# Performance work log

Hardware: AMD Instinct MI355X
Metric: run time of the kernel (lower is better)

The kernel has to match this reference:

```python
import jax, jax.numpy as jnp
import numpy as np

D = 256          # d_embed
KD = 256         # key_d_embed
NHEAD = 8
DK = D // NHEAD  # 32
QH = QW = 128
QWS = 16
KH = KW = 64
KWS = 8
R = QWS // KWS   # qk_ratio = 2
SCALE = 1.0 / np.sqrt(DK)


def _rel_index():
    # query coords on fine grid, key coords scaled up by ratio R
    qc = np.stack(np.meshgrid(np.arange(QWS), np.arange(QWS), indexing='ij'), -1).reshape(-1, 2)
    kc = np.stack(np.meshgrid(np.arange(KWS), np.arange(KWS), indexing='ij'), -1).reshape(-1, 2) * R
    rel = qc[:, None, :] - kc[None, :, :] + (QWS - R)  # values in [0, 2*QWS-R-1]
    return jnp.asarray(rel[..., 0] * (2 * QWS - R) + rel[..., 1])  # (QWS^2, KWS^2)


def _partition(t, ws):
    # (B, h, H, W, d) -> (B, h, H/ws, W/ws, ws*ws, d)
    B, h, H, W, d = t.shape
    t = t.reshape(B, h, H // ws, ws, W // ws, ws, d).transpose(0, 1, 2, 4, 3, 5, 6)
    return t.reshape(B, h, H // ws, W // ws, ws * ws, d)


def _merge(t, ws, H, W):
    # inverse of _partition
    B, h, nH, nW, _, d = t.shape
    t = t.reshape(B, h, nH, nW, ws, ws, d).transpose(0, 1, 2, 4, 3, 5, 6)
    return t.reshape(B, h, H, W, d)


def setup_inputs() -> dict:
    key = jax.random.key(0)
    ks = jax.random.split(key, 9)
    x = jax.random.normal(ks[0], (8, QH, QW, D), dtype=jnp.float32)
    z = jax.random.normal(ks[1], (8, KH, KW, KD), dtype=jnp.float32)
    mask = jax.random.randint(ks[2], (1, NHEAD, QH // QWS, QW // QWS, QWS * QWS, KWS * KWS), 0, 2) == 1
    Wq = jax.random.normal(ks[3], (D, D), dtype=jnp.float32) * 0.02
    bq = jnp.zeros((D,), dtype=jnp.float32)
    Wkv = jax.random.normal(ks[4], (KD, 2 * D), dtype=jnp.float32) * 0.02
    bkv = jnp.zeros((2 * D,), dtype=jnp.float32)
    Wo = jax.random.normal(ks[5], (D, D), dtype=jnp.float32) * 0.02
    bo = jnp.zeros((D,), dtype=jnp.float32)
    rel_table = jax.random.normal(ks[6], ((2 * QWS - R) ** 2, NHEAD), dtype=jnp.float32) * 0.02
    return {"x": x, "z": z, "mask": mask, "Wq": Wq, "bq": bq, "Wkv": Wkv, "bkv": bkv, "Wo": Wo, "bo": bo, "rel_table": rel_table}


def reference(x, z, mask, Wq, bq, Wkv, bkv, Wo, bo, rel_table):
    B, H, W, _ = x.shape
    q = (x @ Wq + bq).reshape(B, H, W, NHEAD, DK).transpose(0, 3, 1, 2, 4)        # (B,h,H,W,dk)
    kv = (z @ Wkv + bkv).reshape(B, KH, KW, 2, NHEAD, DK).transpose(3, 0, 4, 1, 2, 5)
    k, v = kv[0], kv[1]                                                           # (B,h,_H,_W,dk)
    sq, sk = QWS // 2, KWS // 2
    q = jnp.roll(q, (-sq, -sq), axis=(2, 3))
    k = jnp.roll(k, (-sk, -sk), axis=(2, 3))
    v = jnp.roll(v, (-sk, -sk), axis=(2, 3))
    q = _partition(q, QWS)   # (B,h,nh,nw,QWS^2,dk)
    k = _partition(k, KWS)   # (B,h,nh,nw,KWS^2,dk)
    v = _partition(v, KWS)
    attn = jnp.einsum('bhnmqd,bhnmkd->bhnmqk', q, k) * SCALE
    bias = rel_table[_rel_index()].transpose(2, 0, 1)[None, :, None, None]        # (1,h,1,1,QWS^2,KWS^2)
    attn = attn + bias
    attn = jnp.where(mask, jnp.float32(-1e9), attn)
    attn = jax.nn.softmax(attn, axis=-1)
    out = jnp.einsum('bhnmqk,bhnmkd->bhnmqd', attn, v)
    out = _merge(out, QWS, H, W)
    out = jnp.roll(out, (sq, sq), axis=(2, 3))
    out = out.transpose(0, 2, 3, 1, 4).reshape(B, H, W, D)
    return out @ Wo + bo
```

## Files before the change

### kernel.cpp

```cpp
#include <hip/hip_runtime.h>
#include <hip/hip_bf16.h>
#include <type_traits>


typedef __attribute__((ext_vector_type(8))) short short8v;
typedef __attribute__((ext_vector_type(4))) float f32x4;
typedef __attribute__((ext_vector_type(8))) unsigned short ushort8v;
typedef __attribute__((ext_vector_type(4))) unsigned short ushort4v;

#define DEV __device__ __forceinline__

DEV unsigned short f2bf(float f) {
    union { float f; unsigned u; } v; v.f = f;
    unsigned r = v.u + 0x7FFFu + ((v.u >> 16) & 1u);
    return (unsigned short)(r >> 16);
}

#define ATT_SCALE 0.17677669529663687f

__global__ void prep_weights(const float* __restrict__ Wq, const float* __restrict__ Wkv,
                             const float* __restrict__ Wo,
                             unsigned short* __restrict__ WqT, unsigned short* __restrict__ WkvT,
                             unsigned short* __restrict__ WoT) {
    int idx = blockIdx.x * 256 + threadIdx.x;
    if (idx < 65536) {
        int n = idx >> 8, k = idx & 255;
        WqT[idx] = f2bf(Wq[k * 256 + n] * ATT_SCALE);
    } else if (idx < 196608) {
        int i = idx - 65536;
        int n = i >> 8, k = i & 255;
        WkvT[i] = f2bf(Wkv[k * 512 + n]);
    } else {
        int i = idx - 196608;
        int n = i >> 8, k = i & 255;
        WoT[i] = f2bf(Wo[k * 256 + n]);
    }
}

__global__ void prep_bias(const float* __restrict__ rel_table, const float* __restrict__ bq,
                          float* __restrict__ biasb, float* __restrict__ bqs) {
    int idx = blockIdx.x * 256 + threadIdx.x;
    if (idx < 131072) {
        int head = idx >> 14;
        int q = (idx >> 6) & 255;
        int k = idx & 63;
        int qi = q >> 4, qj = q & 15;
        int ki = k >> 3, kj = k & 7;
        int r0 = qi - 2 * ki + 14, r1 = qj - 2 * kj + 14;
        biasb[idx] = rel_table[(r0 * 30 + r1) * 8 + head];
    } else if (idx < 131328) {
        int i = idx - 131072;
        bqs[i] = bq[i] * ATT_SCALE;
    }
}

__global__ void prep_mask(const int* __restrict__ mask, unsigned long long* __restrict__ mp) {
    int idx = blockIdx.x * 256 + threadIdx.x;
    const int4* src = reinterpret_cast<const int4*>(mask + (size_t)idx * 64);
    unsigned long long bits = 0;
#pragma unroll
    for (int c = 0; c < 16; ++c) {
        int4 v = src[c];
        if (v.x) bits |= 1ull << (c * 4 + 0);
        if (v.y) bits |= 1ull << (c * 4 + 1);
        if (v.z) bits |= 1ull << (c * 4 + 2);
        if (v.w) bits |= 1ull << (c * 4 + 3);
    }
    mp[idx] = bits;
}

template <bool AF32, bool OUT_BF16>
__global__ __launch_bounds__(256) void gemm_proj(
    const void* __restrict__ Ain, const unsigned short* __restrict__ BT,
    const float* __restrict__ bias, void* __restrict__ Cout,
    int M, int N, int K)
{
    __shared__ __align__(16) unsigned char As[2][8192];
    __shared__ __align__(16) unsigned char Bs[2][8192];
    const float* Af = (const float*)Ain;
    const unsigned short* Ab = (const unsigned short*)Ain;

    const int tid = threadIdx.x;
    const int mb = blockIdx.y * 128, nb = blockIdx.x * 128;
    const int w = tid >> 6, lane = tid & 63, lr = lane & 15, lg = lane >> 4;
    const int wm = (w >> 1) * 64, wn = (w & 1) * 64;

    const int cr0 = (w << 5) + (lane >> 2);
    const int csp = lane & 3;
    const int cs0 = csp ^ ((cr0 >> 1) & 3);
    const int cs1 = csp ^ (((cr0 + 16) >> 1) & 3);

    auto stageB = [&](int buf, int kb) {
        __builtin_amdgcn_global_load_lds(
            (const __attribute__((address_space(1))) void*)(BT + (size_t)(nb + cr0) * K + kb + cs0 * 8),
            (__attribute__((address_space(3))) void*)(&Bs[buf][w << 11]), 16, 0, 0);
        __builtin_amdgcn_global_load_lds(
            (const __attribute__((address_space(1))) void*)(BT + (size_t)(nb + cr0 + 16) * K + kb + cs1 * 8),
            (__attribute__((address_space(3))) void*)(&Bs[buf][(w << 11) + 1024]), 16, 0, 0);
    };
    auto stageA_lds = [&](int buf, int kb) {
        __builtin_amdgcn_global_load_lds(
            (const __attribute__((address_space(1))) void*)(Ab + (size_t)(mb + cr0) * K + kb + cs0 * 8),
            (__attribute__((address_space(3))) void*)(&As[buf][w << 11]), 16, 0, 0);
        __builtin_amdgcn_global_load_lds(
            (const __attribute__((address_space(1))) void*)(Ab + (size_t)(mb + cr0 + 16) * K + kb + cs1 * 8),
            (__attribute__((address_space(3))) void*)(&As[buf][(w << 11) + 1024]), 16, 0, 0);
    };

    float4 areg[2][2];
    auto loadA = [&](int kb) {
#pragma unroll
        for (int i = 0; i < 2; ++i) {
            int flat = tid + (i << 8);
            int r = flat >> 2, sp = flat & 3;
            int s = sp ^ ((r >> 1) & 3);
            const float* src = Af + (size_t)(mb + r) * K + kb + s * 8;
            areg[i][0] = *reinterpret_cast<const float4*>(src);
            areg[i][1] = *reinterpret_cast<const float4*>(src + 4);
        }
    };
    auto writeA = [&](int buf) {
#pragma unroll
        for (int i = 0; i < 2; ++i) {
            int flat = tid + (i << 8);
            int r = flat >> 2, sp = flat & 3;
            ushort8v u = { f2bf(areg[i][0].x), f2bf(areg[i][0].y),
                           f2bf(areg[i][0].z), f2bf(areg[i][0].w),
                           f2bf(areg[i][1].x), f2bf(areg[i][1].y),
                           f2bf(areg[i][1].z), f2bf(areg[i][1].w) };
            *reinterpret_cast<ushort8v*>(&As[buf][r * 64 + sp * 16]) = u;
        }
    };

    auto rdA = [&](int buf, int row) -> short8v {
        int swz = (lg ^ ((row >> 1) & 3)) << 4;
        return *reinterpret_cast<const short8v*>(&As[buf][row * 64 + swz]);
    };
    auto rdB = [&](int buf, int row) -> short8v {
        int swz = (lg ^ ((row >> 1) & 3)) << 4;
        return *reinterpret_cast<const short8v*>(&Bs[buf][row * 64 + swz]);
    };

    f32x4 acc[4][4];
#pragma unroll
    for (int i = 0; i < 4; ++i)
#pragma unroll
        for (int j = 0; j < 4; ++j) acc[i][j] = {0.f, 0.f, 0.f, 0.f};

    if constexpr (AF32) { loadA(0); stageB(0, 0); writeA(0); }
    else               { stageA_lds(0, 0); stageB(0, 0); }
    __syncthreads();

    const int NT = K >> 5;
    int cur = 0;
    for (int t = 0; t < NT; ++t) {
        if (t + 1 < NT) {
            if constexpr (AF32) { loadA((t + 1) << 5); stageB(cur ^ 1, (t + 1) << 5); }
            else { stageA_lds(cur ^ 1, (t + 1) << 5); stageB(cur ^ 1, (t + 1) << 5); }
        }
        short8v af[4], bfr[4];
#pragma unroll
        for (int mt = 0; mt < 4; ++mt) af[mt] = rdA(cur, wm + mt * 16 + lr);
#pragma unroll
        for (int nt = 0; nt < 4; ++nt) bfr[nt] = rdB(cur, wn + nt * 16 + lr);
#pragma unroll
        for (int mt = 0; mt < 4; ++mt)
#pragma unroll
            for (int nt = 0; nt < 4; ++nt)
                acc[mt][nt] = __builtin_amdgcn_mfma_f32_16x16x32_bf16(
                    af[mt], bfr[nt], acc[mt][nt], 0, 0, 0);
        if (t + 1 < NT) { if constexpr (AF32) writeA(cur ^ 1); }
        __syncthreads();
        cur ^= 1;
    }

#pragma unroll
    for (int mt = 0; mt < 4; ++mt)
#pragma unroll
        for (int nt = 0; nt < 4; ++nt)
#pragma unroll
            for (int j = 0; j < 4; ++j) {
                int row = mb + wm + mt * 16 + lg * 4 + j;
                int col = nb + wn + nt * 16 + lr;
                float v = acc[mt][nt][j] + bias[col];
                if constexpr (OUT_BF16)
                    ((unsigned short*)Cout)[(size_t)row * N + col] = f2bf(v);
                else
                    ((float*)Cout)[(size_t)row * N + col] = v;
            }
}

__global__ __launch_bounds__(256) void win_attn(
    unsigned short* __restrict__ Qbuf,
    const unsigned short* __restrict__ KVbuf,
    const unsigned long long* __restrict__ maskp,
    const float* __restrict__ biasb)
{
    __shared__ __align__(16) unsigned char Pb[256 * 128];
    __shared__ __align__(16) unsigned short Vt[32][72];

    const int tid = threadIdx.x;
    const int win = blockIdx.x, head = blockIdx.y, b = blockIdx.z;
    const int wi = win >> 3, wj = win & 7;
    const int w = tid >> 6, lane = tid & 63, lr = lane & 15, lg = lane >> 4;
    const int qb = w * 64;

    {
        int key = tid & 63, c = tid >> 6;
        int kr = (wi * 8 + (key >> 3) + 4) & 63;
        int kc = (wj * 8 + (key & 7) + 4) & 63;
        ushort8v v = *reinterpret_cast<const ushort8v*>(
            KVbuf + ((size_t)(b * 4096 + kr * 64 + kc)) * 512 + 256 + head * 32 + c * 8);
#pragma unroll
        for (int e = 0; e < 8; ++e) Vt[c * 8 + e][key] = v[e];
    }

    short8v qf[4], kf[4];
#pragma unroll
    for (int mt = 0; mt < 4; ++mt) {
        int q = qb + mt * 16 + lr;
        int gr = (wi * 16 + (q >> 4) + 8) & 127;
        int gc = (wj * 16 + (q & 15) + 8) & 127;
        qf[mt] = *reinterpret_cast<const short8v*>(
            Qbuf + ((size_t)(b * 16384 + gr * 128 + gc)) * 256 + head * 32 + lg * 8);
    }
#pragma unroll
    for (int nt = 0; nt < 4; ++nt) {
        int key = nt * 16 + lr;
        int kr = (wi * 8 + (key >> 3) + 4) & 63;
        int kc = (wj * 8 + (key & 7) + 4) & 63;
        kf[nt] = *reinterpret_cast<const short8v*>(
            KVbuf + ((size_t)(b * 4096 + kr * 64 + kc)) * 512 + head * 32 + lg * 8);
    }

    f32x4 s[4][4];
#pragma unroll
    for (int mt = 0; mt < 4; ++mt)
#pragma unroll
        for (int nt = 0; nt < 4; ++nt) s[mt][nt] = {0.f, 0.f, 0.f, 0.f};
    __builtin_amdgcn_s_setprio(1);
#pragma unroll
    for (int mt = 0; mt < 4; ++mt)
#pragma unroll
        for (int nt = 0; nt < 4; ++nt)
            s[mt][nt] = __builtin_amdgcn_mfma_f32_16x16x32_bf16(qf[mt], kf[nt], s[mt][nt], 0, 0, 0);
    __builtin_amdgcn_s_setprio(0);

    const unsigned long long* mrow = maskp + (size_t)(head * 64 + win) * 256;
#pragma unroll
    for (int mt = 0; mt < 4; ++mt) {
#pragma unroll
        for (int j = 0; j < 4; ++j) {
            int q = qb + mt * 16 + lg * 4 + j;
            unsigned long long mb = mrow[q];
            const float* brow = biasb + (size_t)(head * 256 + q) * 64;
            float v[4];
            float m = -3.0e38f;
#pragma unroll
            for (int nt = 0; nt < 4; ++nt) {
                int key = nt * 16 + lr;
                float sv = s[mt][nt][j] + brow[key];
                if ((mb >> key) & 1ull) sv = -1.0e9f;
                v[nt] = sv;
                m = fmaxf(m, sv);
            }
#pragma unroll
            for (int d = 1; d < 16; d <<= 1) m = fmaxf(m, __shfl_xor(m, d, 64));
            float sum = 0.f;
#pragma unroll
            for (int nt = 0; nt < 4; ++nt) { v[nt] = __expf(v[nt] - m); sum += v[nt]; }
#pragma unroll
            for (int d = 1; d < 16; d <<= 1) sum += __shfl_xor(sum, d, 64);
            float inv = 1.0f / sum;
            int sw = (q & 7) << 4;
#pragma unroll
            for (int nt = 0; nt < 4; ++nt) {
                int off = q * 128 + (((nt * 16 + lr) * 2) ^ sw);
                *reinterpret_cast<unsigned short*>(Pb + off) = f2bf(v[nt] * inv);
            }
        }
    }

    __syncthreads();

    f32x4 o[4][2];
#pragma unroll
    for (int mt = 0; mt < 4; ++mt)
#pragma unroll
        for (int nt = 0; nt < 2; ++nt) o[mt][nt] = {0.f, 0.f, 0.f, 0.f};
#pragma unroll
    for (int kc = 0; kc < 2; ++kc) {
        short8v pf[4], vf[2];
#pragma unroll
        for (int mt = 0; mt < 4; ++mt) {
            int row = qb + mt * 16 + lr;
            int coff = (kc * 64 + lg * 16) ^ ((row & 7) << 4);
            pf[mt] = *reinterpret_cast<const short8v*>(Pb + row * 128 + coff);
        }
#pragma unroll
        for (int nt = 0; nt < 2; ++nt)
            vf[nt] = *reinterpret_cast<const short8v*>(&Vt[nt * 16 + lr][kc * 32 + lg * 8]);
        __builtin_amdgcn_s_setprio(1);
#pragma unroll
        for (int mt = 0; mt < 4; ++mt)
#pragma unroll
            for (int nt = 0; nt < 2; ++nt)
                o[mt][nt] = __builtin_amdgcn_mfma_f32_16x16x32_bf16(pf[mt], vf[nt], o[mt][nt], 0, 0, 0);
        __builtin_amdgcn_s_setprio(0);
    }

#pragma unroll
    for (int mt = 0; mt < 4; ++mt)
#pragma unroll
        for (int j = 0; j < 4; ++j) {
            int q = qb + mt * 16 + lg * 4 + j;
            int gr = (wi * 16 + (q >> 4) + 8) & 127;
            int gc = (wj * 16 + (q & 15) + 8) & 127;
            unsigned short* dst =
                Qbuf + ((size_t)(b * 16384 + gr * 128 + gc)) * 256 + head * 32;
#pragma unroll
            for (int nt = 0; nt < 2; ++nt)
                dst[nt * 16 + lr] = f2bf(o[mt][nt][j]);
        }
}

extern "C" void kernel_launch(void* const* d_in, const int* in_sizes, int n_in,
                              void* d_out, int out_size, void* d_ws, size_t ws_size,
                              hipStream_t stream) {
    const float* x    = (const float*)d_in[0];
    const float* z    = (const float*)d_in[1];
    const int*   mask = (const int*)d_in[2];
    const float* Wq   = (const float*)d_in[3];
    const float* bq   = (const float*)d_in[4];
    const float* Wkv  = (const float*)d_in[5];
    const float* bkv  = (const float*)d_in[6];
    const float* Wo   = (const float*)d_in[7];
    const float* bo   = (const float*)d_in[8];
    const float* rel  = (const float*)d_in[9];
    float* out = (float*)d_out;

    char* ws = (char*)d_ws;
    unsigned short*     Qbuf  = (unsigned short*)(ws);
    unsigned short*     KVbuf = (unsigned short*)(ws + 67108864);
    unsigned short*     WqT   = (unsigned short*)(ws + 100663296);
    unsigned short*     WkvT  = (unsigned short*)(ws + 100794368);
    unsigned short*     WoT   = (unsigned short*)(ws + 101056512);
    float*              biasb = (float*)(ws + 101187584);
    unsigned long long* maskp = (unsigned long long*)(ws + 101711872);
    float*              bqs   = (float*)(ws + 102760448);

    prep_weights<<<1024, 256, 0, stream>>>(Wq, Wkv, Wo, WqT, WkvT, WoT);
    prep_bias<<<513, 256, 0, stream>>>(rel, bq, biasb, bqs);
    prep_mask<<<512, 256, 0, stream>>>(mask, maskp);

    gemm_proj<true, true><<<dim3(2, 1024), 256, 0, stream>>>(
        (const void*)x, WqT, bqs, (void*)Qbuf, 131072, 256, 256);
    gemm_proj<true, true><<<dim3(4, 256), 256, 0, stream>>>(
        (const void*)z, WkvT, bkv, (void*)KVbuf, 32768, 512, 256);
    win_attn<<<dim3(64, 8, 8), 256, 0, stream>>>(Qbuf, KVbuf, maskp, biasb);
    gemm_proj<false, false><<<dim3(2, 1024), 256, 0, stream>>>(
        (const void*)Qbuf, WoT, bo, (void*)out, 131072, 256, 256);
}
```

Before: 221.3 us.

## Fuse Q projection, window attention and output projection into one kernel

```diff
diff --git a/kernel.cpp b/kernel.cpp
--- a/kernel.cpp
+++ b/kernel.cpp
@@ -7,6 +7,7 @@
 typedef __attribute__((ext_vector_type(4))) float f32x4;
 typedef __attribute__((ext_vector_type(8))) unsigned short ushort8v;
 typedef __attribute__((ext_vector_type(4))) unsigned short ushort4v;
+typedef unsigned long long u64;
 
 #define DEV __device__ __forceinline__
 
@@ -14,6 +15,22 @@
     union { float f; unsigned u; } v; v.f = f;
     unsigned r = v.u + 0x7FFFu + ((v.u >> 16) & 1u);
     return (unsigned short)(r >> 16);
+}
+
+DEV short8v cvt_f32x8(const float4 lo, const float4 hi) {
+    union U { __hip_bfloat162 h[4]; short8v s; } u;
+    u.h[0] = __float22bfloat162_rn(float2{lo.x, lo.y});
+    u.h[1] = __float22bfloat162_rn(float2{lo.z, lo.w});
+    u.h[2] = __float22bfloat162_rn(float2{hi.x, hi.y});
+    u.h[3] = __float22bfloat162_rn(float2{hi.z, hi.w});
+    return u.s;
+}
+
+DEV uint2 pack4(f32x4 v) {
+    union { __hip_bfloat162 h; unsigned u; } a, b;
+    a.h = __float22bfloat162_rn(float2{v[0], v[1]});
+    b.h = __float22bfloat162_rn(float2{v[2], v[3]});
+    return uint2{a.u, b.u};
 }
 
 #define ATT_SCALE 0.17677669529663687f
@@ -54,10 +71,10 @@
     }
 }
 
-__global__ void prep_mask(const int* __restrict__ mask, unsigned long long* __restrict__ mp) {
+__global__ void prep_mask(const int* __restrict__ mask, u64* __restrict__ mp) {
     int idx = blockIdx.x * 256 + threadIdx.x;
     const int4* src = reinterpret_cast<const int4*>(mask + (size_t)idx * 64);
-    unsigned long long bits = 0;
+    u64 bits = 0;
 #pragma unroll
     for (int c = 0; c < 16; ++c) {
         int4 v = src[c];
@@ -69,16 +86,13 @@
     mp[idx] = bits;
 }
 
-template <bool AF32, bool OUT_BF16>
-__global__ __launch_bounds__(256) void gemm_proj(
-    const void* __restrict__ Ain, const unsigned short* __restrict__ BT,
-    const float* __restrict__ bias, void* __restrict__ Cout,
+__global__ __launch_bounds__(256) void gemm_kv(
+    const float* __restrict__ Af, const unsigned short* __restrict__ BT,
+    const float* __restrict__ bias, unsigned short* __restrict__ Cout,
     int M, int N, int K)
 {
     __shared__ __align__(16) unsigned char As[2][8192];
     __shared__ __align__(16) unsigned char Bs[2][8192];
-    const float* Af = (const float*)Ain;
-    const unsigned short* Ab = (const unsigned short*)Ain;
 
     const int tid = threadIdx.x;
     const int mb = blockIdx.y * 128, nb = blockIdx.x * 128;
@@ -98,14 +112,6 @@
             (const __attribute__((address_space(1))) void*)(BT + (size_t)(nb + cr0 + 16) * K + kb + cs1 * 8),
             (__attribute__((address_space(3))) void*)(&Bs[buf][(w << 11) + 1024]), 16, 0, 0);
     };
-    auto stageA_lds = [&](int buf, int kb) {
-        __builtin_amdgcn_global_load_lds(
-            (const __attribute__((address_space(1))) void*)(Ab + (size_t)(mb + cr0) * K + kb + cs0 * 8),
-            (__attribute__((address_space(3))) void*)(&As[buf][w << 11]), 16, 0, 0);
-        __builtin_amdgcn_global_load_lds(
-            (const __attribute__((address_space(1))) void*)(Ab + (size_t)(mb + cr0 + 16) * K + kb + cs1 * 8),
-            (__attribute__((address_space(3))) void*)(&As[buf][(w << 11) + 1024]), 16, 0, 0);
-    };
 
     float4 areg[2][2];
     auto loadA = [&](int kb) {
@@ -131,7 +137,6 @@
             *reinterpret_cast<ushort8v*>(&As[buf][r * 64 + sp * 16]) = u;
         }
     };
-
     auto rdA = [&](int buf, int row) -> short8v {
         int swz = (lg ^ ((row >> 1) & 3)) << 4;
         return *reinterpret_cast<const short8v*>(&As[buf][row * 64 + swz]);
@@ -147,17 +152,13 @@
 #pragma unroll
         for (int j = 0; j < 4; ++j) acc[i][j] = {0.f, 0.f, 0.f, 0.f};
 
-    if constexpr (AF32) { loadA(0); stageB(0, 0); writeA(0); }
-    else               { stageA_lds(0, 0); stageB(0, 0); }
+    loadA(0); stageB(0, 0); writeA(0);
     __syncthreads();
 
     const int NT = K >> 5;
     int cur = 0;
     for (int t = 0; t < NT; ++t) {
-        if (t + 1 < NT) {
-            if constexpr (AF32) { loadA((t + 1) << 5); stageB(cur ^ 1, (t + 1) << 5); }
-            else { stageA_lds(cur ^ 1, (t + 1) << 5); stageB(cur ^ 1, (t + 1) << 5); }
-        }
+        if (t + 1 < NT) { loadA((t + 1) << 5); stageB(cur ^ 1, (t + 1) << 5); }
         short8v af[4], bfr[4];
 #pragma unroll
         for (int mt = 0; mt < 4; ++mt) af[mt] = rdA(cur, wm + mt * 16 + lr);
@@ -169,7 +170,7 @@
             for (int nt = 0; nt < 4; ++nt)
                 acc[mt][nt] = __builtin_amdgcn_mfma_f32_16x16x32_bf16(
                     af[mt], bfr[nt], acc[mt][nt], 0, 0, 0);
-        if (t + 1 < NT) { if constexpr (AF32) writeA(cur ^ 1); }
+        if (t + 1 < NT) writeA(cur ^ 1);
         __syncthreads();
         cur ^= 1;
     }
@@ -182,146 +183,204 @@
             for (int j = 0; j < 4; ++j) {
                 int row = mb + wm + mt * 16 + lg * 4 + j;
                 int col = nb + wn + nt * 16 + lr;
-                float v = acc[mt][nt][j] + bias[col];
-                if constexpr (OUT_BF16)
-                    ((unsigned short*)Cout)[(size_t)row * N + col] = f2bf(v);
-                else
-                    ((float*)Cout)[(size_t)row * N + col] = v;
+                Cout[(size_t)row * N + col] = f2bf(acc[mt][nt][j] + bias[col]);
             }
 }
 
-__global__ __launch_bounds__(256) void win_attn(
-    unsigned short* __restrict__ Qbuf,
-    const unsigned short* __restrict__ KVbuf,
-    const unsigned long long* __restrict__ maskp,
-    const float* __restrict__ biasb)
+__global__ __launch_bounds__(256, 2) void fused_attn(
+    const float* __restrict__ x, const unsigned short* __restrict__ KVbuf,
+    const unsigned short* __restrict__ WqT, const unsigned short* __restrict__ WoT,
+    const float* __restrict__ bqs, const float* __restrict__ bo,
+    const u64* __restrict__ maskp, const float* __restrict__ biasb,
+    float* __restrict__ out)
 {
-    __shared__ __align__(16) unsigned char Pb[256 * 128];
-    __shared__ __align__(16) unsigned short Vt[32][72];
+    __shared__ __align__(16) unsigned char L[73728];
 
     const int tid = threadIdx.x;
-    const int win = blockIdx.x, head = blockIdx.y, b = blockIdx.z;
+    const int w = tid >> 6, lane = tid & 63, lr = lane & 15, lg = lane >> 4;
+    const int qblk = blockIdx.x, win = blockIdx.y, b = blockIdx.z;
     const int wi = win >> 3, wj = win & 7;
-    const int w = tid >> 6, lane = tid & 63, lr = lane & 15, lg = lane >> 4;
-    const int qb = w * 64;
 
     {
         int key = tid & 63, c = tid >> 6;
         int kr = (wi * 8 + (key >> 3) + 4) & 63;
         int kc = (wj * 8 + (key & 7) + 4) & 63;
-        ushort8v v = *reinterpret_cast<const ushort8v*>(
-            KVbuf + ((size_t)(b * 4096 + kr * 64 + kc)) * 512 + 256 + head * 32 + c * 8);
-#pragma unroll
-        for (int e = 0; e < 8; ++e) Vt[c * 8 + e][key] = v[e];
-    }
-
-    short8v qf[4], kf[4];
-#pragma unroll
-    for (int mt = 0; mt < 4; ++mt) {
-        int q = qb + mt * 16 + lr;
-        int gr = (wi * 16 + (q >> 4) + 8) & 127;
-        int gc = (wj * 16 + (q & 15) + 8) & 127;
-        qf[mt] = *reinterpret_cast<const short8v*>(
-            Qbuf + ((size_t)(b * 16384 + gr * 128 + gc)) * 256 + head * 32 + lg * 8);
-    }
+        const unsigned short* vsrc =
+            KVbuf + ((size_t)(b * 4096 + kr * 64 + kc)) * 512 + 256 + c * 64;
+        unsigned char* vt = L + 32768 + (key >> 5) * 16384;
+        const int klby = (key & 31) * 2;
+#pragma unroll
+        for (int i = 0; i < 8; ++i) {
+            ushort8v v = *reinterpret_cast<const ushort8v*>(vsrc + i * 8);
+#pragma unroll
+            for (int e = 0; e < 8; ++e) {
+                int d = c * 64 + i * 8 + e;
+                *reinterpret_cast<unsigned short*>(
+                    vt + d * 64 + (klby ^ (((d >> 1) & 3) << 4))) = (unsigned short)v[e];
+            }
+        }
+    }
+
+    f32x4 acc[16];
+#pragma unroll
+    for (int i = 0; i < 16; ++i) acc[i] = {0.f, 0.f, 0.f, 0.f};
+
+    const unsigned short* wqb = WqT + (size_t)(w * 64 + lr) * 256 + lg * 8;
+    const float* xr[4];
+#pragma unroll
+    for (int qt = 0; qt < 4; ++qt) {
+        int gr = (wi * 16 + qblk * 4 + qt + 8) & 127;
+        int gc = (wj * 16 + lr + 8) & 127;
+        xr[qt] = x + ((size_t)((b * 128 + gr) * 128 + gc)) * 256 + lg * 8;
+    }
+#pragma unroll
+    for (int kt = 0; kt < 8; ++kt) {
+        short8v wqf[4], xf[4];
+#pragma unroll
+        for (int nt = 0; nt < 4; ++nt)
+            wqf[nt] = *reinterpret_cast<const short8v*>(wqb + nt * 4096 + kt * 32);
+#pragma unroll
+        for (int qt = 0; qt < 4; ++qt) {
+            float4 lo = *reinterpret_cast<const float4*>(xr[qt] + kt * 32);
+            float4 hi = *reinterpret_cast<const float4*>(xr[qt] + kt * 32 + 4);
+            xf[qt] = cvt_f32x8(lo, hi);
+        }
+#pragma unroll
+        for (int nt = 0; nt < 4; ++nt)
+#pragma unroll
+            for (int qt = 0; qt < 4; ++qt)
+                acc[nt * 4 + qt] = __builtin_amdgcn_mfma_f32_16x16x32_bf16(
+                    wqf[nt], xf[qt], acc[nt * 4 + qt], 0, 0, 0);
+    }
+#pragma unroll
+    for (int nt = 0; nt < 4; ++nt) {
+        int n0 = w * 64 + nt * 16 + lg * 4;
+        f32x4 bq4 = *reinterpret_cast<const f32x4*>(bqs + n0);
+        unsigned char* pl = L + (w * 2 + (nt >> 1)) * 4096;
+        int cby = (nt & 1) * 32 + lg * 8;
+#pragma unroll
+        for (int qt = 0; qt < 4; ++qt) {
+            int qr = qt * 16 + lr;
+            uint2 pk = pack4(acc[nt * 4 + qt] + bq4);
+            *reinterpret_cast<uint2*>(pl + qr * 64 + (cby ^ (((qr >> 1) & 3) << 4))) = pk;
+        }
+    }
+    __syncthreads();
+
+    const int qrow = w * 16 + lr;
+    const int qg = qblk * 64 + qrow;
+    const int swzq = ((qrow >> 1) & 3) << 4;
+    const unsigned short* kp[4];
 #pragma unroll
     for (int nt = 0; nt < 4; ++nt) {
         int key = nt * 16 + lr;
         int kr = (wi * 8 + (key >> 3) + 4) & 63;
         int kc = (wj * 8 + (key & 7) + 4) & 63;
-        kf[nt] = *reinterpret_cast<const short8v*>(
-            KVbuf + ((size_t)(b * 4096 + kr * 64 + kc)) * 512 + head * 32 + lg * 8);
-    }
-
-    f32x4 s[4][4];
-#pragma unroll
-    for (int mt = 0; mt < 4; ++mt)
-#pragma unroll
-        for (int nt = 0; nt < 4; ++nt) s[mt][nt] = {0.f, 0.f, 0.f, 0.f};
-    __builtin_amdgcn_s_setprio(1);
-#pragma unroll
-    for (int mt = 0; mt < 4; ++mt)
-#pragma unroll
-        for (int nt = 0; nt < 4; ++nt)
-            s[mt][nt] = __builtin_amdgcn_mfma_f32_16x16x32_bf16(qf[mt], kf[nt], s[mt][nt], 0, 0, 0);
-    __builtin_amdgcn_s_setprio(0);
-
-    const unsigned long long* mrow = maskp + (size_t)(head * 64 + win) * 256;
-#pragma unroll
-    for (int mt = 0; mt < 4; ++mt) {
-#pragma unroll
-        for (int j = 0; j < 4; ++j) {
-            int q = qb + mt * 16 + lg * 4 + j;
-            unsigned long long mb = mrow[q];
-            const float* brow = biasb + (size_t)(head * 256 + q) * 64;
-            float v[4];
-            float m = -3.0e38f;
-#pragma unroll
-            for (int nt = 0; nt < 4; ++nt) {
-                int key = nt * 16 + lr;
-                float sv = s[mt][nt][j] + brow[key];
-                if ((mb >> key) & 1ull) sv = -1.0e9f;
-                v[nt] = sv;
+        kp[nt] = KVbuf + ((size_t)(b * 4096 + kr * 64 + kc)) * 512 + lg * 8;
+    }
+    const float* bb = biasb + (size_t)qg * 64 + lg * 4;
+    const u64* mrow = maskp + (size_t)win * 256 + qg;
+
+#pragma unroll
+    for (int h = 0; h < 8; ++h) {
+        short8v qf = *reinterpret_cast<const short8v*>(
+            L + h * 4096 + qrow * 64 + ((lg << 4) ^ swzq));
+        f32x4 s[4];
+#pragma unroll
+        for (int nt = 0; nt < 4; ++nt) {
+            short8v kf = *reinterpret_cast<const short8v*>(kp[nt] + h * 32);
+            f32x4 z = {0.f, 0.f, 0.f, 0.f};
+            s[nt] = __builtin_amdgcn_mfma_f32_16x16x32_bf16(kf, qf, z, 0, 0, 0);
+        }
+        u64 mb = mrow[(size_t)h * 16384];
+        float vv[16];
+        float m = -3.0e38f;
+#pragma unroll
+        for (int nt = 0; nt < 4; ++nt) {
+            f32x4 b4 = *reinterpret_cast<const f32x4*>(bb + h * 16384 + nt * 16);
+#pragma unroll
+            for (int j = 0; j < 4; ++j) {
+                float sv = s[nt][j] + b4[j];
+                if ((mb >> (nt * 16 + lg * 4 + j)) & 1ull) sv = -1.0e9f;
+                vv[nt * 4 + j] = sv;
                 m = fmaxf(m, sv);
             }
-#pragma unroll
-            for (int d = 1; d < 16; d <<= 1) m = fmaxf(m, __shfl_xor(m, d, 64));
-            float sum = 0.f;
-#pragma unroll
-            for (int nt = 0; nt < 4; ++nt) { v[nt] = __expf(v[nt] - m); sum += v[nt]; }
-#pragma unroll
-            for (int d = 1; d < 16; d <<= 1) sum += __shfl_xor(sum, d, 64);
-            float inv = 1.0f / sum;
-            int sw = (q & 7) << 4;
-#pragma unroll
-            for (int nt = 0; nt < 4; ++nt) {
-                int off = q * 128 + (((nt * 16 + lr) * 2) ^ sw);
-                *reinterpret_cast<unsigned short*>(Pb + off) = f2bf(v[nt] * inv);
+        }
+        m = fmaxf(m, __shfl_xor(m, 16, 64));
+        m = fmaxf(m, __shfl_xor(m, 32, 64));
+        float sum = 0.f;
+#pragma unroll
+        for (int i = 0; i < 16; ++i) { vv[i] = __expf(vv[i] - m); sum += vv[i]; }
+        sum += __shfl_xor(sum, 16, 64);
+        sum += __shfl_xor(sum, 32, 64);
+        float inv = 1.0f / sum;
+#pragma unroll
+        for (int nt = 0; nt < 4; ++nt) {
+            f32x4 pv = { vv[nt * 4 + 0] * inv, vv[nt * 4 + 1] * inv,
+                         vv[nt * 4 + 2] * inv, vv[nt * 4 + 3] * inv };
+            uint2 pk = pack4(pv);
+            *reinterpret_cast<uint2*>(
+                L + 65536 + (nt >> 1) * 4096 + qrow * 64 +
+                ((((nt & 1) * 32 + lg * 8)) ^ swzq)) = pk;
+        }
+        f32x4 o[2];
+        o[0] = {0.f, 0.f, 0.f, 0.f}; o[1] = {0.f, 0.f, 0.f, 0.f};
+#pragma unroll
+        for (int kcp = 0; kcp < 2; ++kcp) {
+            short8v pf = *reinterpret_cast<const short8v*>(
+                L + 65536 + kcp * 4096 + qrow * 64 + ((lg << 4) ^ swzq));
+#pragma unroll
+            for (int nt2 = 0; nt2 < 2; ++nt2) {
+                int d = h * 32 + nt2 * 16 + lr;
+                short8v vf = *reinterpret_cast<const short8v*>(
+                    L + 32768 + kcp * 16384 + d * 64 + ((lg << 4) ^ (((d >> 1) & 3) << 4)));
+                o[nt2] = __builtin_amdgcn_mfma_f32_16x16x32_bf16(vf, pf, o[nt2], 0, 0, 0);
             }
         }
-    }
-
+#pragma unroll
+        for (int nt2 = 0; nt2 < 2; ++nt2) {
+            uint2 pk = pack4(o[nt2]);
+            *reinterpret_cast<uint2*>(
+                L + h * 4096 + qrow * 64 + ((nt2 * 32 + lg * 8) ^ swzq)) = pk;
+        }
+    }
     __syncthreads();
 
-    f32x4 o[4][2];
-#pragma unroll
-    for (int mt = 0; mt < 4; ++mt)
-#pragma unroll
-        for (int nt = 0; nt < 2; ++nt) o[mt][nt] = {0.f, 0.f, 0.f, 0.f};
-#pragma unroll
-    for (int kc = 0; kc < 2; ++kc) {
-        short8v pf[4], vf[2];
-#pragma unroll
-        for (int mt = 0; mt < 4; ++mt) {
-            int row = qb + mt * 16 + lr;
-            int coff = (kc * 64 + lg * 16) ^ ((row & 7) << 4);
-            pf[mt] = *reinterpret_cast<const short8v*>(Pb + row * 128 + coff);
-        }
-#pragma unroll
-        for (int nt = 0; nt < 2; ++nt)
-            vf[nt] = *reinterpret_cast<const short8v*>(&Vt[nt * 16 + lr][kc * 32 + lg * 8]);
-        __builtin_amdgcn_s_setprio(1);
-#pragma unroll
-        for (int mt = 0; mt < 4; ++mt)
-#pragma unroll
-            for (int nt = 0; nt < 2; ++nt)
-                o[mt][nt] = __builtin_amdgcn_mfma_f32_16x16x32_bf16(pf[mt], vf[nt], o[mt][nt], 0, 0, 0);
-        __builtin_amdgcn_s_setprio(0);
-    }
-
-#pragma unroll
-    for (int mt = 0; mt < 4; ++mt)
-#pragma unroll
-        for (int j = 0; j < 4; ++j) {
-            int q = qb + mt * 16 + lg * 4 + j;
-            int gr = (wi * 16 + (q >> 4) + 8) & 127;
-            int gc = (wj * 16 + (q & 15) + 8) & 127;
-            unsigned short* dst =
-                Qbuf + ((size_t)(b * 16384 + gr * 128 + gc)) * 256 + head * 32;
-#pragma unroll
-            for (int nt = 0; nt < 2; ++nt)
-                dst[nt * 16 + lr] = f2bf(o[mt][nt][j]);
-        }
+#pragma unroll
+    for (int i = 0; i < 16; ++i) acc[i] = {0.f, 0.f, 0.f, 0.f};
+    const unsigned short* wob = WoT + (size_t)(w * 64 + lr) * 256 + lg * 8;
+#pragma unroll
+    for (int kt = 0; kt < 8; ++kt) {
+        short8v wof[4], of[4];
+#pragma unroll
+        for (int nt = 0; nt < 4; ++nt)
+            wof[nt] = *reinterpret_cast<const short8v*>(wob + nt * 4096 + kt * 32);
+#pragma unroll
+        for (int qt = 0; qt < 4; ++qt) {
+            int qr = qt * 16 + lr;
+            of[qt] = *reinterpret_cast<const short8v*>(
+                L + kt * 4096 + qr * 64 + ((lg << 4) ^ (((qr >> 1) & 3) << 4)));
+        }
+#pragma unroll
+        for (int nt = 0; nt < 4; ++nt)
+#pragma unroll
+            for (int qt = 0; qt < 4; ++qt)
+                acc[nt * 4 + qt] = __builtin_amdgcn_mfma_f32_16x16x32_bf16(
+                    wof[nt], of[qt], acc[nt * 4 + qt], 0, 0, 0);
+    }
+#pragma unroll
+    for (int nt = 0; nt < 4; ++nt) {
+        int n0 = w * 64 + nt * 16 + lg * 4;
+        f32x4 bo4 = *reinterpret_cast<const f32x4*>(bo + n0);
+#pragma unroll
+        for (int qt = 0; qt < 4; ++qt) {
+            int gr = (wi * 16 + qblk * 4 + qt + 8) & 127;
+            int gc = (wj * 16 + lr + 8) & 127;
+            f32x4 v = acc[nt * 4 + qt] + bo4;
+            *reinterpret_cast<f32x4*>(
+                out + ((size_t)((b * 128 + gr) * 128 + gc)) * 256 + n0) = v;
+        }
+    }
 }
 
 extern "C" void kernel_launch(void* const* d_in, const int* in_sizes, int n_in,
@@ -340,24 +399,20 @@
     float* out = (float*)d_out;
 
     char* ws = (char*)d_ws;
-    unsigned short*     Qbuf  = (unsigned short*)(ws);
-    unsigned short*     KVbuf = (unsigned short*)(ws + 67108864);
-    unsigned short*     WqT   = (unsigned short*)(ws + 100663296);
-    unsigned short*     WkvT  = (unsigned short*)(ws + 100794368);
-    unsigned short*     WoT   = (unsigned short*)(ws + 101056512);
-    float*              biasb = (float*)(ws + 101187584);
-    unsigned long long* maskp = (unsigned long long*)(ws + 101711872);
-    float*              bqs   = (float*)(ws + 102760448);
+    unsigned short* KVbuf = (unsigned short*)(ws);
+    unsigned short* WqT   = (unsigned short*)(ws + 33554432);
+    unsigned short* WkvT  = (unsigned short*)(ws + 33685504);
+    unsigned short* WoT   = (unsigned short*)(ws + 33947648);
+    float*          biasb = (float*)(ws + 34078720);
+    u64*            maskp = (u64*)(ws + 34603008);
+    float*          bqs   = (float*)(ws + 35651584);
 
     prep_weights<<<1024, 256, 0, stream>>>(Wq, Wkv, Wo, WqT, WkvT, WoT);
     prep_bias<<<513, 256, 0, stream>>>(rel, bq, biasb, bqs);
     prep_mask<<<512, 256, 0, stream>>>(mask, maskp);
 
-    gemm_proj<true, true><<<dim3(2, 1024), 256, 0, stream>>>(
-        (const void*)x, WqT, bqs, (void*)Qbuf, 131072, 256, 256);
-    gemm_proj<true, true><<<dim3(4, 256), 256, 0, stream>>>(
-        (const void*)z, WkvT, bkv, (void*)KVbuf, 32768, 512, 256);
-    win_attn<<<dim3(64, 8, 8), 256, 0, stream>>>(Qbuf, KVbuf, maskp, biasb);
-    gemm_proj<false, false><<<dim3(2, 1024), 256, 0, stream>>>(
-        (const void*)Qbuf, WoT, bo, (void*)out, 131072, 256, 256);
-}
+    gemm_kv<<<dim3(4, 256), 256, 0, stream>>>(z, WkvT, bkv, KVbuf, 32768, 512, 256);
+
+    fused_attn<<<dim3(4, 64, 8), 256, 0, stream>>>(
+        x, KVbuf, WqT, WoT, bqs, bo, maskp, biasb, out);
+}
```

Result: slower. 264.8 us (+19.7%).

## Keep full weight matrix resident in LDS for Q and output projections

Applied to the files above, without the earlier changes.

```diff
diff --git a/kernel.cpp b/kernel.cpp
--- a/kernel.cpp
+++ b/kernel.cpp
@@ -7,6 +7,7 @@
 typedef __attribute__((ext_vector_type(4))) float f32x4;
 typedef __attribute__((ext_vector_type(8))) unsigned short ushort8v;
 typedef __attribute__((ext_vector_type(4))) unsigned short ushort4v;
+typedef unsigned long long u64;
 
 #define DEV __device__ __forceinline__
 
@@ -14,6 +15,15 @@
     union { float f; unsigned u; } v; v.f = f;
     unsigned r = v.u + 0x7FFFu + ((v.u >> 16) & 1u);
     return (unsigned short)(r >> 16);
+}
+
+DEV short8v cvt_f32x8(const float4 lo, const float4 hi) {
+    union U { __hip_bfloat162 h[4]; short8v s; } u;
+    u.h[0] = __float22bfloat162_rn(float2{lo.x, lo.y});
+    u.h[1] = __float22bfloat162_rn(float2{lo.z, lo.w});
+    u.h[2] = __float22bfloat162_rn(float2{hi.x, hi.y});
+    u.h[3] = __float22bfloat162_rn(float2{hi.z, hi.w});
+    return u.s;
 }
 
 #define ATT_SCALE 0.17677669529663687f
@@ -54,10 +64,10 @@
     }
 }
 
-__global__ void prep_mask(const int* __restrict__ mask, unsigned long long* __restrict__ mp) {
+__global__ void prep_mask(const int* __restrict__ mask, u64* __restrict__ mp) {
     int idx = blockIdx.x * 256 + threadIdx.x;
     const int4* src = reinterpret_cast<const int4*>(mask + (size_t)idx * 64);
-    unsigned long long bits = 0;
+    u64 bits = 0;
 #pragma unroll
     for (int c = 0; c < 16; ++c) {
         int4 v = src[c];
@@ -67,6 +77,120 @@
         if (v.w) bits |= 1ull << (c * 4 + 3);
     }
     mp[idx] = bits;
+}
+
+template <bool AF32, bool OUT_BF16>
+__global__ __launch_bounds__(512) void gemm_ws(
+    const void* __restrict__ Ain, const unsigned short* __restrict__ BT,
+    const float* __restrict__ bias, void* __restrict__ Cout)
+{
+    __shared__ __align__(16) unsigned char Wl[131072];
+    const float* Af = (const float*)Ain;
+    const unsigned short* Ab = (const unsigned short*)Ain;
+
+    const int tid = threadIdx.x;
+    const int w = tid >> 6, lane = tid & 63, lr = lane & 15, lg = lane >> 4;
+    const size_t wm = (size_t)blockIdx.x * 512 + w * 64;
+
+    {
+        int r = tid >> 1, half = tid & 1;
+        const unsigned short* src = BT + r * 256 + half * 128;
+        int rsw = (r >> 1) & 3;
+#pragma unroll
+        for (int kk = 0; kk < 4; ++kk) {
+            int kt = half * 4 + kk;
+#pragma unroll
+            for (int sl = 0; sl < 4; ++sl) {
+                ushort8v v = *reinterpret_cast<const ushort8v*>(src + kk * 32 + sl * 8);
+                *reinterpret_cast<ushort8v*>(
+                    &Wl[kt * 16384 + r * 64 + ((sl ^ rsw) << 4)]) = v;
+            }
+        }
+    }
+    __syncthreads();
+
+    const int swzb = (lg ^ ((lr >> 1) & 3)) << 4;
+
+    float bcol[16];
+#pragma unroll
+    for (int nt = 0; nt < 16; ++nt) bcol[nt] = bias[nt * 16 + lr];
+
+#define RD_W(kt, nt) (*reinterpret_cast<const short8v*>( \
+        &Wl[(kt) * 16384 + ((nt) * 16 + lr) * 64 + swzb]))
+
+#define EPILOGUE(t)                                                             \
+    _Pragma("unroll")                                                           \
+    for (int nt = 0; nt < 16; ++nt) {                                           \
+        _Pragma("unroll")                                                       \
+        for (int j = 0; j < 4; ++j) {                                           \
+            size_t row = wm + (t) * 16 + lg * 4 + j;                            \
+            int col = nt * 16 + lr;                                             \
+            float v = acc[nt][j] + bcol[nt];                                    \
+            if constexpr (OUT_BF16)                                             \
+                ((unsigned short*)Cout)[row * 256 + col] = f2bf(v);             \
+            else                                                                \
+                ((float*)Cout)[row * 256 + col] = v;                            \
+        }                                                                       \
+    }
+
+    if constexpr (AF32) {
+        float4 bufA[16], bufB[16];
+#define LOADT_F(BUF, t) {                                                       \
+        const float* p = Af + (wm + (t) * 16 + lr) * 256 + lg * 8;              \
+        _Pragma("unroll")                                                       \
+        for (int kt = 0; kt < 8; ++kt) {                                        \
+            BUF[kt * 2]     = *reinterpret_cast<const float4*>(p + kt * 32);    \
+            BUF[kt * 2 + 1] = *reinterpret_cast<const float4*>(p + kt * 32 + 4);\
+        } }
+#define COMP_F(BUF, t) {                                                        \
+        f32x4 acc[16];                                                          \
+        _Pragma("unroll")                                                       \
+        for (int nt = 0; nt < 16; ++nt) acc[nt] = {0.f, 0.f, 0.f, 0.f};         \
+        _Pragma("unroll")                                                       \
+        for (int kt = 0; kt < 8; ++kt) {                                        \
+            short8v a = cvt_f32x8(BUF[kt * 2], BUF[kt * 2 + 1]);                \
+            _Pragma("unroll")                                                   \
+            for (int nt = 0; nt < 16; ++nt)                                     \
+                acc[nt] = __builtin_amdgcn_mfma_f32_16x16x32_bf16(              \
+                    a, RD_W(kt, nt), acc[nt], 0, 0, 0);                         \
+        }                                                                       \
+        EPILOGUE(t) }
+        LOADT_F(bufA, 0);
+        LOADT_F(bufB, 1); COMP_F(bufA, 0);
+        LOADT_F(bufA, 2); COMP_F(bufB, 1);
+        LOADT_F(bufB, 3); COMP_F(bufA, 2);
+        COMP_F(bufB, 3);
+#undef LOADT_F
+#undef COMP_F
+    } else {
+        short8v bufA[8], bufB[8];
+#define LOADT_B(BUF, t) {                                                       \
+        const unsigned short* p = Ab + (wm + (t) * 16 + lr) * 256 + lg * 8;     \
+        _Pragma("unroll")                                                       \
+        for (int kt = 0; kt < 8; ++kt)                                          \
+            BUF[kt] = *reinterpret_cast<const short8v*>(p + kt * 32); }
+#define COMP_B(BUF, t) {                                                        \
+        f32x4 acc[16];                                                          \
+        _Pragma("unroll")                                                       \
+        for (int nt = 0; nt < 16; ++nt) acc[nt] = {0.f, 0.f, 0.f, 0.f};         \
+        _Pragma("unroll")                                                       \
+        for (int kt = 0; kt < 8; ++kt) {                                        \
+            _Pragma("unroll")                                                   \
+            for (int nt = 0; nt < 16; ++nt)                                     \
+                acc[nt] = __builtin_amdgcn_mfma_f32_16x16x32_bf16(              \
+                    BUF[kt], RD_W(kt, nt), acc[nt], 0, 0, 0);                   \
+        }                                                                       \
+        EPILOGUE(t) }
+        LOADT_B(bufA, 0);
+        LOADT_B(bufB, 1); COMP_B(bufA, 0);
+        LOADT_B(bufA, 2); COMP_B(bufB, 1);
+        LOADT_B(bufB, 3); COMP_B(bufA, 2);
+        COMP_B(bufB, 3);
+#undef LOADT_B
+#undef COMP_B
+    }
+#undef RD_W
+#undef EPILOGUE
 }
 
 template <bool AF32, bool OUT_BF16>
@@ -78,7 +202,6 @@
     __shared__ __align__(16) unsigned char As[2][8192];
     __shared__ __align__(16) unsigned char Bs[2][8192];
     const float* Af = (const float*)Ain;
-    const unsigned short* Ab = (const unsigned short*)Ain;
 
     const int tid = threadIdx.x;
     const int mb = blockIdx.y * 128, nb = blockIdx.x * 128;
@@ -98,14 +221,6 @@
             (const __attribute__((address_space(1))) void*)(BT + (size_t)(nb + cr0 + 16) * K + kb + cs1 * 8),
             (__attribute__((address_space(3))) void*)(&Bs[buf][(w << 11) + 1024]), 16, 0, 0);
     };
-    auto stageA_lds = [&](int buf, int kb) {
-        __builtin_amdgcn_global_load_lds(
-            (const __attribute__((address_space(1))) void*)(Ab + (size_t)(mb + cr0) * K + kb + cs0 * 8),
-            (__attribute__((address_space(3))) void*)(&As[buf][w << 11]), 16, 0, 0);
-        __builtin_amdgcn_global_load_lds(
-            (const __attribute__((address_space(1))) void*)(Ab + (size_t)(mb + cr0 + 16) * K + kb + cs1 * 8),
-            (__attribute__((address_space(3))) void*)(&As[buf][(w << 11) + 1024]), 16, 0, 0);
-    };
 
     float4 areg[2][2];
     auto loadA = [&](int kb) {
@@ -131,7 +246,6 @@
             *reinterpret_cast<ushort8v*>(&As[buf][r * 64 + sp * 16]) = u;
         }
     };
-
     auto rdA = [&](int buf, int row) -> short8v {
         int swz = (lg ^ ((row >> 1) & 3)) << 4;
         return *reinterpret_cast<const short8v*>(&As[buf][row * 64 + swz]);
@@ -147,17 +261,13 @@
 #pragma unroll
         for (int j = 0; j < 4; ++j) acc[i][j] = {0.f, 0.f, 0.f, 0.f};
 
-    if constexpr (AF32) { loadA(0); stageB(0, 0); writeA(0); }
-    else               { stageA_lds(0, 0); stageB(0, 0); }
+    loadA(0); stageB(0, 0); writeA(0);
     __syncthreads();
 
     const int NT = K >> 5;
     int cur = 0;
     for (int t = 0; t < NT; ++t) {
-        if (t + 1 < NT) {
-            if constexpr (AF32) { loadA((t + 1) << 5); stageB(cur ^ 1, (t + 1) << 5); }
-            else { stageA_lds(cur ^ 1, (t + 1) << 5); stageB(cur ^ 1, (t + 1) << 5); }
-        }
+        if (t + 1 < NT) { loadA((t + 1) << 5); stageB(cur ^ 1, (t + 1) << 5); }
         short8v af[4], bfr[4];
 #pragma unroll
         for (int mt = 0; mt < 4; ++mt) af[mt] = rdA(cur, wm + mt * 16 + lr);
@@ -169,7 +279,7 @@
             for (int nt = 0; nt < 4; ++nt)
                 acc[mt][nt] = __builtin_amdgcn_mfma_f32_16x16x32_bf16(
                     af[mt], bfr[nt], acc[mt][nt], 0, 0, 0);
-        if (t + 1 < NT) { if constexpr (AF32) writeA(cur ^ 1); }
+        if (t + 1 < NT) writeA(cur ^ 1);
         __syncthreads();
         cur ^= 1;
     }
@@ -193,7 +303,7 @@
 __global__ __launch_bounds__(256) void win_attn(
     unsigned short* __restrict__ Qbuf,
     const unsigned short* __restrict__ KVbuf,
-    const unsigned long long* __restrict__ maskp,
+    const u64* __restrict__ maskp,
     const float* __restrict__ biasb)
 {
     __shared__ __align__(16) unsigned char Pb[256 * 128];
@@ -246,13 +356,13 @@
             s[mt][nt] = __builtin_amdgcn_mfma_f32_16x16x32_bf16(qf[mt], kf[nt], s[mt][nt], 0, 0, 0);
     __builtin_amdgcn_s_setprio(0);
 
-    const unsigned long long* mrow = maskp + (size_t)(head * 64 + win) * 256;
+    const u64* mrow = maskp + (size_t)(head * 64 + win) * 256;
 #pragma unroll
     for (int mt = 0; mt < 4; ++mt) {
 #pragma unroll
         for (int j = 0; j < 4; ++j) {
             int q = qb + mt * 16 + lg * 4 + j;
-            unsigned long long mb = mrow[q];
+            u64 mb = mrow[q];
             const float* brow = biasb + (size_t)(head * 256 + q) * 64;
             float v[4];
             float m = -3.0e38f;
@@ -340,24 +450,24 @@
     float* out = (float*)d_out;
 
     char* ws = (char*)d_ws;
-    unsigned short*     Qbuf  = (unsigned short*)(ws);
-    unsigned short*     KVbuf = (unsigned short*)(ws + 67108864);
-    unsigned short*     WqT   = (unsigned short*)(ws + 100663296);
-    unsigned short*     WkvT  = (unsigned short*)(ws + 100794368);
-    unsigned short*     WoT   = (unsigned short*)(ws + 101056512);
-    float*              biasb = (float*)(ws + 101187584);
-    unsigned long long* maskp = (unsigned long long*)(ws + 101711872);
-    float*              bqs   = (float*)(ws + 102760448);
+    unsigned short* Qbuf  = (unsigned short*)(ws);
+    unsigned short* KVbuf = (unsigned short*)(ws + 67108864);
+    unsigned short* WqT   = (unsigned short*)(ws + 100663296);
+    unsigned short* WkvT  = (unsigned short*)(ws + 100794368);
+    unsigned short* WoT   = (unsigned short*)(ws + 101056512);
+    float*          biasb = (float*)(ws + 101187584);
+    u64*            maskp = (u64*)(ws + 101711872);
+    float*          bqs   = (float*)(ws + 102760448);
 
     prep_weights<<<1024, 256, 0, stream>>>(Wq, Wkv, Wo, WqT, WkvT, WoT);
     prep_bias<<<513, 256, 0, stream>>>(rel, bq, biasb, bqs);
     prep_mask<<<512, 256, 0, stream>>>(mask, maskp);
 
-    gemm_proj<true, true><<<dim3(2, 1024), 256, 0, stream>>>(
-        (const void*)x, WqT, bqs, (void*)Qbuf, 131072, 256, 256);
+    gemm_ws<true, true><<<256, 512, 0, stream>>>(
+        (const void*)x, WqT, bqs, (void*)Qbuf);
     gemm_proj<true, true><<<dim3(4, 256), 256, 0, stream>>>(
         (const void*)z, WkvT, bkv, (void*)KVbuf, 32768, 512, 256);
     win_attn<<<dim3(64, 8, 8), 256, 0, stream>>>(Qbuf, KVbuf, maskp, biasb);
-    gemm_proj<false, false><<<dim3(2, 1024), 256, 0, stream>>>(
-        (const void*)Qbuf, WoT, bo, (void*)out, 131072, 256, 256);
-}
+    gemm_ws<false, false><<<256, 512, 0, stream>>>(
+        (const void*)Qbuf, WoT, bo, (void*)out);
+}
```

Result: no change. 219.5 us (-0.8%).
